# Optimization experiments

Hardware: AMD Instinct MI355X
Metric: run time of the kernel (lower is better)

The kernel has to match this reference:

```python
import jax, jax.numpy as jnp
import numpy as np

B, T, Dx, H, K = 32, 4096, 128, 128, 10


def setup_inputs() -> dict:
    key = jax.random.key(0)
    ks = jax.random.split(key, 11)
    s = 1.0 / np.sqrt(H)  # PyTorch GRU init range

    def p(k, shape):
        return jax.random.uniform(k, shape, jnp.float32, -s, s)

    return {
        "x": jax.random.normal(ks[0], (B, T, Dx), jnp.float32),
        # forward-direction GRU params (gate order: r, z, n as in PyTorch)
        "W_ih_f": p(ks[1], (3 * H, Dx)),
        "W_hh_f": p(ks[2], (3 * H, H)),
        "b_ih_f": p(ks[3], (3 * H,)),
        "b_hh_f": p(ks[4], (3 * H,)),
        # backward-direction GRU params
        "W_ih_b": p(ks[5], (3 * H, Dx)),
        "W_hh_b": p(ks[6], (3 * H, H)),
        "b_ih_b": p(ks[7], (3 * H,)),
        "b_hh_b": p(ks[8], (3 * H,)),
        # final linear classifier
        "W_fc": p(ks[9], (K, 2 * H)),
        "b_fc": p(ks[10], (K,)),
    }


def _gru_scan(x, Wih, Whh, bih, bhh, reverse):
    """Single-direction GRU over time. x: [B,T,Dx] -> [B,T,H]."""
    # Precompute all input projections at once: [T, B, 3H]
    xp = jnp.einsum('btd,gd->tbg', x, Wih) + bih
    Whh_T = Whh.T
    Hd = Whh.shape[1]

    def cell(h, xt):
        hp = h @ Whh_T + bhh            # [B, 3H]
        xr, xz, xn = jnp.split(xt, 3, axis=-1)
        hr, hz, hn = jnp.split(hp, 3, axis=-1)
        r = jax.nn.sigmoid(xr + hr)
        z = jax.nn.sigmoid(xz + hz)
        n = jnp.tanh(xn + r * hn)
        h_new = (1.0 - z) * n + z * h
        return h_new, h_new

    h0 = jnp.zeros((x.shape[0], Hd), x.dtype)
    _, hs = jax.lax.scan(cell, h0, xp, reverse=reverse)  # [T, B, H]
    return jnp.transpose(hs, (1, 0, 2))


def reference(x, W_ih_f, W_hh_f, b_ih_f, b_hh_f,
              W_ih_b, W_hh_b, b_ih_b, b_hh_b, W_fc, b_fc):
    hf = _gru_scan(x, W_ih_f, W_hh_f, b_ih_f, b_hh_f, reverse=False)
    hb = _gru_scan(x, W_ih_b, W_hh_b, b_ih_b, b_hh_b, reverse=True)
    h = jnp.concatenate([hf, hb], axis=-1)  # [B, T, 2H]
    return h @ W_fc.T + b_fc                # [B, T, K]
```

## Files before the change

kernel.cpp:

```cpp
#include <hip/hip_runtime.h>
#include <cstdint>
#include <cstddef>

#define T_LEN   4096
#define B_SZ    32
#define H_DIM   128
#define DX      128
#define K_CLS   10
#define CHUNK   32
#define NCHUNKS (T_LEN / CHUNK)
#define XA_LD   136
#define HIST_LD 136

typedef _Float16 half2v  __attribute__((ext_vector_type(2)));
typedef _Float16 half8   __attribute__((ext_vector_type(8)));
typedef float    floatx4 __attribute__((ext_vector_type(4)));

__device__ __forceinline__ float dot2f(unsigned int w, unsigned int h, float acc) {
  return __builtin_amdgcn_fdot2(__builtin_bit_cast(half2v, w),
                                __builtin_bit_cast(half2v, h), acc, false);
}

__device__ __forceinline__ unsigned int packh2(float a, float b) {
  half2v h;
  h.x = (_Float16)a;
  h.y = (_Float16)b;
  return __builtin_bit_cast(unsigned int, h);
}

__device__ __forceinline__ float dpp_xor1_add(float x) {
  int xi = __builtin_bit_cast(int, x);
  int yi = __builtin_amdgcn_update_dpp(xi, xi, 0xB1, 0xF, 0xF, false);
  return x + __builtin_bit_cast(float, yi);
}

__device__ __forceinline__ float sigm(float x) {
  x = fminf(fmaxf(x, -30.f), 30.f);
  return __builtin_amdgcn_rcpf(1.f + __expf(-x));
}

__device__ __forceinline__ float tanhfast(float x) {
  x = fminf(fmaxf(x, -15.f), 15.f);
  float t = __expf(-2.f * x);
  return (1.f - t) * __builtin_amdgcn_rcpf(1.f + t);
}

__global__ void __launch_bounds__(256) init_out_kernel(float* __restrict__ out,
                                                       const float* __restrict__ bfc) {
  int i = blockIdx.x * 256 + threadIdx.x;
  if (i < B_SZ * T_LEN * K_CLS) out[i] = bfc[i % K_CLS];
}

__global__ void __launch_bounds__(256, 1)
gru_bidir_kernel(const float* __restrict__ x,
                 const float* __restrict__ Wih_f, const float* __restrict__ Whh_f,
                 const float* __restrict__ bih_f, const float* __restrict__ bhh_f,
                 const float* __restrict__ Wih_b, const float* __restrict__ Whh_b,
                 const float* __restrict__ bih_b, const float* __restrict__ bhh_b,
                 const float* __restrict__ Wfc, float* __restrict__ out) {
  const int tid = threadIdx.x;
  const int bid = blockIdx.x;
  const int b   = bid & (B_SZ - 1);
  const int dir = bid >> 5;

  const float* Wih = dir ? Wih_b : Wih_f;
  const float* Whh = dir ? Whh_b : Whh_f;
  const float* bih = dir ? bih_b : bih_f;
  const float* bhh = dir ? bhh_b : bhh_f;

  const int lane = tid & 63;
  const int wv   = tid >> 6;
  const int col  = lane & 15;
  const int quad = lane >> 4;
  const int j    = tid >> 1;
  const int q    = tid & 1;

  __shared__ __align__(16) _Float16 xA[CHUNK][XA_LD];
  __shared__ __align__(16) _Float16 xh2[CHUNK][4 * H_DIM];
  __shared__ __align__(16) _Float16 hist[CHUNK][HIST_LD];
  __shared__ __align__(16) _Float16 hbuf[2][H_DIM];

  unsigned int whr[32], whz[32], whn[32];
  {
    const float* Wr = Whh + (size_t)j * H_DIM + q * 64;
    const float* Wz = Whh + (size_t)(H_DIM + j) * H_DIM + q * 64;
    const float* Wn = Whh + (size_t)(2 * H_DIM + j) * H_DIM + q * 64;
#pragma unroll
    for (int i = 0; i < 32; ++i) {
      whr[i] = packh2(Wr[2 * i], Wr[2 * i + 1]);
      whz[i] = packh2(Wz[2 * i], Wz[2 * i + 1]);
      whn[i] = packh2(Wn[2 * i], Wn[2 * i + 1]);
    }
  }
  const float cbr  = bih[j] + bhh[j];
  const float cbz  = bih[H_DIM + j] + bhh[H_DIM + j];
  const float bin_ = bih[2 * H_DIM + j];
  const float bhn  = bhh[2 * H_DIM + j];

  half8 fcfrag[4];
#pragma unroll
  for (int ks = 0; ks < 4; ++ks) {
    half8 v;
#pragma unroll
    for (int e = 0; e < 8; ++e) {
      int cc = ks * 32 + quad * 8 + e;
      v[e] = (col < K_CLS) ? (_Float16)Wfc[(size_t)col * (2 * H_DIM) + dir * H_DIM + cc]
                           : (_Float16)0.f;
    }
    fcfrag[ks] = v;
  }

  if (tid < 128) hbuf[0][tid] = (_Float16)0.f;

  const int s_row = tid >> 3;
  const int cbase = (tid & 7) * 16;
  float4 px0, px1, px2, px3;
  {
    int t0 = dir ? (T_LEN - 1 - s_row) : s_row;
    const float* xp = x + ((size_t)b * T_LEN + t0) * DX + cbase;
    px0 = *(const float4*)xp;       px1 = *(const float4*)(xp + 4);
    px2 = *(const float4*)(xp + 8); px3 = *(const float4*)(xp + 12);
  }

  float hold = 0.f;
  __syncthreads();

  for (int c = 0; c < NCHUNKS; ++c) {
    {
      half8 lo, hi;
      lo[0] = (_Float16)px0.x; lo[1] = (_Float16)px0.y; lo[2] = (_Float16)px0.z; lo[3] = (_Float16)px0.w;
      lo[4] = (_Float16)px1.x; lo[5] = (_Float16)px1.y; lo[6] = (_Float16)px1.z; lo[7] = (_Float16)px1.w;
      hi[0] = (_Float16)px2.x; hi[1] = (_Float16)px2.y; hi[2] = (_Float16)px2.z; hi[3] = (_Float16)px2.w;
      hi[4] = (_Float16)px3.x; hi[5] = (_Float16)px3.y; hi[6] = (_Float16)px3.z; hi[7] = (_Float16)px3.w;
      *(half8*)&xA[s_row][cbase] = lo;
      *(half8*)&xA[s_row][cbase + 8] = hi;
    }
    __syncthreads();

#pragma unroll
    for (int nt = 0; nt < 6; ++nt) {
      const int g = (wv * 6 + nt) * 16 + col;
      const float* wsrc = Wih + (size_t)g * DX + quad * 8;
      half8 bf[4];
#pragma unroll
      for (int ks = 0; ks < 4; ++ks) {
        const float* s8 = wsrc + ks * 32;
        half8 v;
#pragma unroll
        for (int e = 0; e < 8; ++e) v[e] = (_Float16)s8[e];
        bf[ks] = v;
      }
      floatx4 a0 = (floatx4){0.f, 0.f, 0.f, 0.f};
      floatx4 a1 = (floatx4){0.f, 0.f, 0.f, 0.f};
#pragma unroll
      for (int ks = 0; ks < 4; ++ks) {
        half8 af0 = *(const half8*)&xA[col][ks * 32 + quad * 8];
        half8 af1 = *(const half8*)&xA[16 + col][ks * 32 + quad * 8];
        a0 = __builtin_amdgcn_mfma_f32_16x16x32_f16(af0, bf[ks], a0, 0, 0, 0);
        a1 = __builtin_amdgcn_mfma_f32_16x16x32_f16(af1, bf[ks], a1, 0, 0, 0);
      }
      const int jj = (g & 127) * 4 + (g >> 7);
#pragma unroll
      for (int i = 0; i < 4; ++i) {
        xh2[quad * 4 + i][jj]      = (_Float16)a0[i];
        xh2[16 + quad * 4 + i][jj] = (_Float16)a1[i];
      }
    }

    if (c + 1 < NCHUNKS) {
      int s = (c + 1) * CHUNK + s_row;
      int t0 = dir ? (T_LEN - 1 - s) : s;
      const float* xp = x + ((size_t)b * T_LEN + t0) * DX + cbase;
      px0 = *(const float4*)xp;       px1 = *(const float4*)(xp + 4);
      px2 = *(const float4*)(xp + 8); px3 = *(const float4*)(xp + 12);
    }
    __syncthreads();

    int p = 0;
#pragma unroll 2
    for (int s = 0; s < CHUNK; ++s) {
      const uint2 xv = *(const uint2*)&xh2[s][j * 4];
      const uint4* hb = (const uint4*)&hbuf[p][q * 64];
      uint4 h0 = hb[0], h1 = hb[1], h2 = hb[2], h3 = hb[3];
      uint4 h4 = hb[4], h5 = hb[5], h6 = hb[6], h7 = hb[7];
      unsigned int hh[32];
      hh[0]=h0.x;  hh[1]=h0.y;  hh[2]=h0.z;  hh[3]=h0.w;
      hh[4]=h1.x;  hh[5]=h1.y;  hh[6]=h1.z;  hh[7]=h1.w;
      hh[8]=h2.x;  hh[9]=h2.y;  hh[10]=h2.z; hh[11]=h2.w;
      hh[12]=h3.x; hh[13]=h3.y; hh[14]=h3.z; hh[15]=h3.w;
      hh[16]=h4.x; hh[17]=h4.y; hh[18]=h4.z; hh[19]=h4.w;
      hh[20]=h5.x; hh[21]=h5.y; hh[22]=h5.z; hh[23]=h5.w;
      hh[24]=h6.x; hh[25]=h6.y; hh[26]=h6.z; hh[27]=h6.w;
      hh[28]=h7.x; hh[29]=h7.y; hh[30]=h7.z; hh[31]=h7.w;

      float ar0 = 0.f, ar1 = 0.f, az0 = 0.f, az1 = 0.f, an0 = 0.f, an1 = 0.f;
#pragma unroll
      for (int i = 0; i < 16; ++i) {
        ar0 = dot2f(whr[2 * i],     hh[2 * i],     ar0);
        ar1 = dot2f(whr[2 * i + 1], hh[2 * i + 1], ar1);
        az0 = dot2f(whz[2 * i],     hh[2 * i],     az0);
        az1 = dot2f(whz[2 * i + 1], hh[2 * i + 1], az1);
        an0 = dot2f(whn[2 * i],     hh[2 * i],     an0);
        an1 = dot2f(whn[2 * i + 1], hh[2 * i + 1], an1);
      }
      float ar = dpp_xor1_add(ar0 + ar1);
      float az = dpp_xor1_add(az0 + az1);
      float an = dpp_xor1_add(an0 + an1);

      half2v x01 = __builtin_bit_cast(half2v, xv.x);
      half2v x23 = __builtin_bit_cast(half2v, xv.y);
      float rr = sigm((float)x01.x + cbr + ar);
      float zz = sigm((float)x01.y + cbz + az);
      float nn = tanhfast((float)x23.x + bin_ + rr * (an + bhn));
      hold = nn + zz * (hold - nn);

      if (q == 0) {
        _Float16 hf = (_Float16)hold;
        hbuf[p ^ 1][j] = hf;
        hist[s][j] = hf;
      }
      p ^= 1;
      __syncthreads();
    }

    if (wv < 2) {
      const int mt = wv;
      floatx4 facc = (floatx4){0.f, 0.f, 0.f, 0.f};
#pragma unroll
      for (int ks = 0; ks < 4; ++ks) {
        half8 af = *(const half8*)&hist[mt * 16 + col][ks * 32 + quad * 8];
        facc = __builtin_amdgcn_mfma_f32_16x16x32_f16(af, fcfrag[ks], facc, 0, 0, 0);
      }
      if (col < K_CLS) {
#pragma unroll
        for (int i = 0; i < 4; ++i) {
          int s = mt * 16 + quad * 4 + i;
          int t = c * CHUNK + s;
          int tt = dir ? (T_LEN - 1 - t) : t;
          atomicAdd(out + ((size_t)b * T_LEN + tt) * K_CLS + col, facc[i]);
        }
      }
    }
  }
}

extern "C" void kernel_launch(void* const* d_in, const int* in_sizes, int n_in,
                              void* d_out, int out_size, void* d_ws, size_t ws_size,
                              hipStream_t stream) {
  (void)in_sizes; (void)n_in; (void)d_ws; (void)ws_size; (void)out_size;
  const float* x     = (const float*)d_in[0];
  const float* Wih_f = (const float*)d_in[1];
  const float* Whh_f = (const float*)d_in[2];
  const float* bih_f = (const float*)d_in[3];
  const float* bhh_f = (const float*)d_in[4];
  const float* Wih_b = (const float*)d_in[5];
  const float* Whh_b = (const float*)d_in[6];
  const float* bih_b = (const float*)d_in[7];
  const float* bhh_b = (const float*)d_in[8];
  const float* Wfc   = (const float*)d_in[9];
  const float* bfc   = (const float*)d_in[10];
  float* out = (float*)d_out;

  const int n_out = B_SZ * T_LEN * K_CLS;
  init_out_kernel<<<(n_out + 255) / 256, 256, 0, stream>>>(out, bfc);
  gru_bidir_kernel<<<B_SZ * 2, 256, 0, stream>>>(x, Wih_f, Whh_f, bih_f, bhh_f,
                                                 Wih_b, Whh_b, bih_b, bhh_b, Wfc, out);
}
```

Baseline: 2.008 ms.

## Process four batch rows per block with interleaved recurrence steps

Each workgroup now carries four batch sequences of one direction (16 blocks instead of 64), with the time chunk cut from 32 to 8. Within each time step the four independent GRU updates are interleaved, so their dot products and LDS loads can hide each other's latency, and one barrier per step is shared by four sequences. A separate pre-kernel converts W_ih to fp16 once in the workspace so the chunk projection loads half-precision weights directly. Barriers are replaced by an explicit lgkmcnt wait plus s_barrier. The trade-off is four times the serial work per step on far fewer compute units.

```diff
diff --git a/kernel.cpp b/kernel.cpp
--- a/kernel.cpp
+++ b/kernel.cpp
@@ -7,10 +7,13 @@
 #define H_DIM   128
 #define DX      128
 #define K_CLS   10
-#define CHUNK   32
+#define G       4
+#define CHUNK   8
+#define NROW    (G * CHUNK)
 #define NCHUNKS (T_LEN / CHUNK)
 #define XA_LD   136
-#define HIST_LD 136
+#define HI_LD   136
+#define XH_W    520
 
 typedef _Float16 half2v  __attribute__((ext_vector_type(2)));
 typedef _Float16 half8   __attribute__((ext_vector_type(8)));
@@ -45,40 +48,56 @@
   return (1.f - t) * __builtin_amdgcn_rcpf(1.f + t);
 }
 
+__device__ __forceinline__ void bar_lgkm() {
+  asm volatile("s_waitcnt lgkmcnt(0)\n\ts_barrier" ::: "memory");
+}
+
 __global__ void __launch_bounds__(256) init_out_kernel(float* __restrict__ out,
                                                        const float* __restrict__ bfc) {
   int i = blockIdx.x * 256 + threadIdx.x;
   if (i < B_SZ * T_LEN * K_CLS) out[i] = bfc[i % K_CLS];
 }
 
+__global__ void __launch_bounds__(256) cvt_wih_kernel(const float* __restrict__ a,
+                                                      const float* __restrict__ b,
+                                                      _Float16* __restrict__ oa,
+                                                      _Float16* __restrict__ ob) {
+  int i = blockIdx.x * 256 + threadIdx.x;
+  if (i < 3 * H_DIM * DX) {
+    oa[i] = (_Float16)a[i];
+    ob[i] = (_Float16)b[i];
+  }
+}
+
 __global__ void __launch_bounds__(256, 1)
 gru_bidir_kernel(const float* __restrict__ x,
-                 const float* __restrict__ Wih_f, const float* __restrict__ Whh_f,
-                 const float* __restrict__ bih_f, const float* __restrict__ bhh_f,
-                 const float* __restrict__ Wih_b, const float* __restrict__ Whh_b,
-                 const float* __restrict__ bih_b, const float* __restrict__ bhh_b,
+                 const float* __restrict__ Whh_f, const float* __restrict__ bih_f,
+                 const float* __restrict__ bhh_f,
+                 const float* __restrict__ Whh_b, const float* __restrict__ bih_b,
+                 const float* __restrict__ bhh_b,
+                 const _Float16* __restrict__ wih16_f, const _Float16* __restrict__ wih16_b,
                  const float* __restrict__ Wfc, float* __restrict__ out) {
   const int tid = threadIdx.x;
   const int bid = blockIdx.x;
-  const int b   = bid & (B_SZ - 1);
-  const int dir = bid >> 5;
-
-  const float* Wih = dir ? Wih_b : Wih_f;
+  const int dir = bid >> 3;
+  const int b0  = (bid & 7) * G;
+
   const float* Whh = dir ? Whh_b : Whh_f;
   const float* bih = dir ? bih_b : bih_f;
   const float* bhh = dir ? bhh_b : bhh_f;
-
-  const int lane = tid & 63;
-  const int wv   = tid >> 6;
-  const int col  = lane & 15;
-  const int quad = lane >> 4;
-  const int j    = tid >> 1;
-  const int q    = tid & 1;
-
-  __shared__ __align__(16) _Float16 xA[CHUNK][XA_LD];
-  __shared__ __align__(16) _Float16 xh2[CHUNK][4 * H_DIM];
-  __shared__ __align__(16) _Float16 hist[CHUNK][HIST_LD];
-  __shared__ __align__(16) _Float16 hbuf[2][H_DIM];
+  const _Float16* Wih16 = dir ? wih16_b : wih16_f;
+
+  const int lane  = tid & 63;
+  const int wv    = tid >> 6;
+  const int mcol  = lane & 15;
+  const int mquad = lane >> 4;
+  const int j     = tid >> 1;
+  const int q     = tid & 1;
+
+  __shared__ __align__(16) _Float16 xAf[NROW * XA_LD];
+  __shared__ __align__(16) _Float16 xh2f[NROW * XH_W];
+  __shared__ __align__(16) _Float16 histf[NROW * HI_LD];
+  __shared__ __align__(16) _Float16 hbuf[2][G][H_DIM];
 
   unsigned int whr[32], whz[32], whn[32];
   {
@@ -103,124 +122,148 @@
     half8 v;
 #pragma unroll
     for (int e = 0; e < 8; ++e) {
-      int cc = ks * 32 + quad * 8 + e;
-      v[e] = (col < K_CLS) ? (_Float16)Wfc[(size_t)col * (2 * H_DIM) + dir * H_DIM + cc]
-                           : (_Float16)0.f;
+      int cc = ks * 32 + mquad * 8 + e;
+      v[e] = (mcol < K_CLS) ? (_Float16)Wfc[(size_t)mcol * (2 * H_DIM) + dir * H_DIM + cc]
+                            : (_Float16)0.f;
     }
     fcfrag[ks] = v;
   }
 
-  if (tid < 128) hbuf[0][tid] = (_Float16)0.f;
-
-  const int s_row = tid >> 3;
+  if (tid < 128) {
+#pragma unroll
+    for (int c = 0; c < G; ++c) hbuf[0][c][tid] = (_Float16)0.f;
+  }
+
+  const int prow  = tid >> 3;
+  const int pc    = prow >> 3;
+  const int ps    = prow & 7;
   const int cbase = (tid & 7) * 16;
   float4 px0, px1, px2, px3;
   {
-    int t0 = dir ? (T_LEN - 1 - s_row) : s_row;
-    const float* xp = x + ((size_t)b * T_LEN + t0) * DX + cbase;
+    int t0 = dir ? (T_LEN - 1 - ps) : ps;
+    const float* xp = x + ((size_t)(b0 + pc) * T_LEN + t0) * DX + cbase;
     px0 = *(const float4*)xp;       px1 = *(const float4*)(xp + 4);
     px2 = *(const float4*)(xp + 8); px3 = *(const float4*)(xp + 12);
   }
 
-  float hold = 0.f;
+  float hold0 = 0.f, hold1 = 0.f, hold2 = 0.f, hold3 = 0.f;
+  int p = 0;
   __syncthreads();
 
-  for (int c = 0; c < NCHUNKS; ++c) {
+  auto ldhh = [&](int c, uint4* h) {
+    const uint4* hb = (const uint4*)&hbuf[p][c][q * 64];
+#pragma unroll
+    for (int i = 0; i < 8; ++i) h[i] = hb[i];
+  };
+  auto ldxv = [&](int c, int s) -> uint2 {
+    return *(const uint2*)&xh2f[(size_t)(c * CHUNK + s) * XH_W + j * 4];
+  };
+  auto stepc = [&](int c, int s, const uint4* hv, uint2 xv, float hold) -> float {
+    unsigned int hh[32];
+#pragma unroll
+    for (int i = 0; i < 8; ++i) {
+      hh[4 * i]     = hv[i].x;
+      hh[4 * i + 1] = hv[i].y;
+      hh[4 * i + 2] = hv[i].z;
+      hh[4 * i + 3] = hv[i].w;
+    }
+    float ar0 = 0.f, ar1 = 0.f, az0 = 0.f, az1 = 0.f, an0 = 0.f, an1 = 0.f;
+#pragma unroll
+    for (int i = 0; i < 16; ++i) {
+      ar0 = dot2f(whr[2 * i],     hh[2 * i],     ar0);
+      ar1 = dot2f(whr[2 * i + 1], hh[2 * i + 1], ar1);
+      az0 = dot2f(whz[2 * i],     hh[2 * i],     az0);
+      az1 = dot2f(whz[2 * i + 1], hh[2 * i + 1], az1);
+      an0 = dot2f(whn[2 * i],     hh[2 * i],     an0);
+      an1 = dot2f(whn[2 * i + 1], hh[2 * i + 1], an1);
+    }
+    float ar = dpp_xor1_add(ar0 + ar1);
+    float az = dpp_xor1_add(az0 + az1);
+    float an = dpp_xor1_add(an0 + an1);
+
+    half2v x01 = __builtin_bit_cast(half2v, xv.x);
+    half2v x23 = __builtin_bit_cast(half2v, xv.y);
+    float rr = sigm((float)x01.x + cbr + ar);
+    float zz = sigm((float)x01.y + cbz + az);
+    float nn = tanhfast((float)x23.x + bin_ + rr * (an + bhn));
+    float hnew = nn + zz * (hold - nn);
+    if (q == 0) {
+      _Float16 hf = (_Float16)hnew;
+      hbuf[p ^ 1][c][j] = hf;
+      histf[(size_t)(c * CHUNK + s) * HI_LD + j] = hf;
+    }
+    return hnew;
+  };
+
+  for (int ck = 0; ck < NCHUNKS; ++ck) {
     {
       half8 lo, hi;
       lo[0] = (_Float16)px0.x; lo[1] = (_Float16)px0.y; lo[2] = (_Float16)px0.z; lo[3] = (_Float16)px0.w;
       lo[4] = (_Float16)px1.x; lo[5] = (_Float16)px1.y; lo[6] = (_Float16)px1.z; lo[7] = (_Float16)px1.w;
       hi[0] = (_Float16)px2.x; hi[1] = (_Float16)px2.y; hi[2] = (_Float16)px2.z; hi[3] = (_Float16)px2.w;
       hi[4] = (_Float16)px3.x; hi[5] = (_Float16)px3.y; hi[6] = (_Float16)px3.z; hi[7] = (_Float16)px3.w;
-      *(half8*)&xA[s_row][cbase] = lo;
-      *(half8*)&xA[s_row][cbase + 8] = hi;
-    }
-    __syncthreads();
-
-#pragma unroll
-    for (int nt = 0; nt < 6; ++nt) {
-      const int g = (wv * 6 + nt) * 16 + col;
-      const float* wsrc = Wih + (size_t)g * DX + quad * 8;
-      half8 bf[4];
-#pragma unroll
-      for (int ks = 0; ks < 4; ++ks) {
-        const float* s8 = wsrc + ks * 32;
-        half8 v;
-#pragma unroll
-        for (int e = 0; e < 8; ++e) v[e] = (_Float16)s8[e];
-        bf[ks] = v;
-      }
-      floatx4 a0 = (floatx4){0.f, 0.f, 0.f, 0.f};
-      floatx4 a1 = (floatx4){0.f, 0.f, 0.f, 0.f};
-#pragma unroll
-      for (int ks = 0; ks < 4; ++ks) {
-        half8 af0 = *(const half8*)&xA[col][ks * 32 + quad * 8];
-        half8 af1 = *(const half8*)&xA[16 + col][ks * 32 + quad * 8];
-        a0 = __builtin_amdgcn_mfma_f32_16x16x32_f16(af0, bf[ks], a0, 0, 0, 0);
-        a1 = __builtin_amdgcn_mfma_f32_16x16x32_f16(af1, bf[ks], a1, 0, 0, 0);
-      }
-      const int jj = (g & 127) * 4 + (g >> 7);
-#pragma unroll
-      for (int i = 0; i < 4; ++i) {
-        xh2[quad * 4 + i][jj]      = (_Float16)a0[i];
-        xh2[16 + quad * 4 + i][jj] = (_Float16)a1[i];
-      }
-    }
-
-    if (c + 1 < NCHUNKS) {
-      int s = (c + 1) * CHUNK + s_row;
-      int t0 = dir ? (T_LEN - 1 - s) : s;
-      const float* xp = x + ((size_t)b * T_LEN + t0) * DX + cbase;
-      px0 = *(const float4*)xp;       px1 = *(const float4*)(xp + 4);
-      px2 = *(const float4*)(xp + 8); px3 = *(const float4*)(xp + 12);
-    }
-    __syncthreads();
-
-    int p = 0;
-#pragma unroll 2
+      *(half8*)&xAf[prow * XA_LD + cbase] = lo;
+      *(half8*)&xAf[prow * XA_LD + cbase + 8] = hi;
+    }
+    bar_lgkm();
+
+    {
+      floatx4 acc[6][2];
+#pragma unroll
+      for (int nt = 0; nt < 6; ++nt) {
+        acc[nt][0] = (floatx4){0.f, 0.f, 0.f, 0.f};
+        acc[nt][1] = (floatx4){0.f, 0.f, 0.f, 0.f};
+      }
+#pragma unroll
+      for (int nt = 0; nt < 6; ++nt) {
+        const int g = (wv * 6 + nt) * 16 + mcol;
+        const _Float16* wsrc = Wih16 + (size_t)g * DX + mquad * 8;
+        half8 bf0 = *(const half8*)(wsrc);
+        half8 bf1 = *(const half8*)(wsrc + 32);
+        half8 bf2 = *(const half8*)(wsrc + 64);
+        half8 bf3 = *(const half8*)(wsrc + 96);
+#pragma unroll
+        for (int mt = 0; mt < 2; ++mt) {
+          const _Float16* ab = &xAf[(mt * 16 + mcol) * XA_LD + mquad * 8];
+          acc[nt][mt] = __builtin_amdgcn_mfma_f32_16x16x32_f16(*(const half8*)(ab),      bf0, acc[nt][mt], 0, 0, 0);
+          acc[nt][mt] = __builtin_amdgcn_mfma_f32_16x16x32_f16(*(const half8*)(ab + 32), bf1, acc[nt][mt], 0, 0, 0);
+          acc[nt][mt] = __builtin_amdgcn_mfma_f32_16x16x32_f16(*(const half8*)(ab + 64), bf2, acc[nt][mt], 0, 0, 0);
+          acc[nt][mt] = __builtin_amdgcn_mfma_f32_16x16x32_f16(*(const half8*)(ab + 96), bf3, acc[nt][mt], 0, 0, 0);
+        }
+      }
+
+      if (ck + 1 < NCHUNKS) {
+        int t = (ck + 1) * CHUNK + ps;
+        int t0 = dir ? (T_LEN - 1 - t) : t;
+        const float* xp = x + ((size_t)(b0 + pc) * T_LEN + t0) * DX + cbase;
+        px0 = *(const float4*)xp;       px1 = *(const float4*)(xp + 4);
+        px2 = *(const float4*)(xp + 8); px3 = *(const float4*)(xp + 12);
+      }
+
+#pragma unroll
+      for (int nt = 0; nt < 6; ++nt) {
+        const int g  = (wv * 6 + nt) * 16 + mcol;
+        const int jj = (g & 127) * 4 + (g >> 7);
+#pragma unroll
+        for (int mt = 0; mt < 2; ++mt)
+#pragma unroll
+          for (int i = 0; i < 4; ++i)
+            xh2f[(size_t)(mt * 16 + mquad * 4 + i) * XH_W + jj] = (_Float16)acc[nt][mt][i];
+      }
+    }
+    bar_lgkm();
+
+#pragma unroll 1
     for (int s = 0; s < CHUNK; ++s) {
-      const uint2 xv = *(const uint2*)&xh2[s][j * 4];
-      const uint4* hb = (const uint4*)&hbuf[p][q * 64];
-      uint4 h0 = hb[0], h1 = hb[1], h2 = hb[2], h3 = hb[3];
-      uint4 h4 = hb[4], h5 = hb[5], h6 = hb[6], h7 = hb[7];
-      unsigned int hh[32];
-      hh[0]=h0.x;  hh[1]=h0.y;  hh[2]=h0.z;  hh[3]=h0.w;
-      hh[4]=h1.x;  hh[5]=h1.y;  hh[6]=h1.z;  hh[7]=h1.w;
-      hh[8]=h2.x;  hh[9]=h2.y;  hh[10]=h2.z; hh[11]=h2.w;
-      hh[12]=h3.x; hh[13]=h3.y; hh[14]=h3.z; hh[15]=h3.w;
-      hh[16]=h4.x; hh[17]=h4.y; hh[18]=h4.z; hh[19]=h4.w;
-      hh[20]=h5.x; hh[21]=h5.y; hh[22]=h5.z; hh[23]=h5.w;
-      hh[24]=h6.x; hh[25]=h6.y; hh[26]=h6.z; hh[27]=h6.w;
-      hh[28]=h7.x; hh[29]=h7.y; hh[30]=h7.z; hh[31]=h7.w;
-
-      float ar0 = 0.f, ar1 = 0.f, az0 = 0.f, az1 = 0.f, an0 = 0.f, an1 = 0.f;
-#pragma unroll
-      for (int i = 0; i < 16; ++i) {
-        ar0 = dot2f(whr[2 * i],     hh[2 * i],     ar0);
-        ar1 = dot2f(whr[2 * i + 1], hh[2 * i + 1], ar1);
-        az0 = dot2f(whz[2 * i],     hh[2 * i],     az0);
-        az1 = dot2f(whz[2 * i + 1], hh[2 * i + 1], az1);
-        an0 = dot2f(whn[2 * i],     hh[2 * i],     an0);
-        an1 = dot2f(whn[2 * i + 1], hh[2 * i + 1], an1);
-      }
-      float ar = dpp_xor1_add(ar0 + ar1);
-      float az = dpp_xor1_add(az0 + az1);
-      float an = dpp_xor1_add(an0 + an1);
-
-      half2v x01 = __builtin_bit_cast(half2v, xv.x);
-      half2v x23 = __builtin_bit_cast(half2v, xv.y);
-      float rr = sigm((float)x01.x + cbr + ar);
-      float zz = sigm((float)x01.y + cbz + az);
-      float nn = tanhfast((float)x23.x + bin_ + rr * (an + bhn));
-      hold = nn + zz * (hold - nn);
-
-      if (q == 0) {
-        _Float16 hf = (_Float16)hold;
-        hbuf[p ^ 1][j] = hf;
-        hist[s][j] = hf;
-      }
+      uint4 hA[8], hB[8];
+      ldhh(0, hA); uint2 xv0 = ldxv(0, s);
+      ldhh(1, hB); uint2 xv1 = ldxv(1, s);
+      hold0 = stepc(0, s, hA, xv0, hold0); ldhh(2, hA); uint2 xv2 = ldxv(2, s);
+      hold1 = stepc(1, s, hB, xv1, hold1); ldhh(3, hB); uint2 xv3 = ldxv(3, s);
+      hold2 = stepc(2, s, hA, xv2, hold2);
+      hold3 = stepc(3, s, hB, xv3, hold3);
       p ^= 1;
-      __syncthreads();
+      bar_lgkm();
     }
 
     if (wv < 2) {
@@ -228,16 +271,17 @@
       floatx4 facc = (floatx4){0.f, 0.f, 0.f, 0.f};
 #pragma unroll
       for (int ks = 0; ks < 4; ++ks) {
-        half8 af = *(const half8*)&hist[mt * 16 + col][ks * 32 + quad * 8];
+        half8 af = *(const half8*)&histf[(size_t)(mt * 16 + mcol) * HI_LD + ks * 32 + mquad * 8];
         facc = __builtin_amdgcn_mfma_f32_16x16x32_f16(af, fcfrag[ks], facc, 0, 0, 0);
       }
-      if (col < K_CLS) {
+      if (mcol < K_CLS) {
 #pragma unroll
         for (int i = 0; i < 4; ++i) {
-          int s = mt * 16 + quad * 4 + i;
-          int t = c * CHUNK + s;
+          int r  = mt * 16 + mquad * 4 + i;
+          int cc = r >> 3, ss = r & 7;
+          int t  = ck * CHUNK + ss;
           int tt = dir ? (T_LEN - 1 - t) : t;
-          atomicAdd(out + ((size_t)b * T_LEN + tt) * K_CLS + col, facc[i]);
+          atomicAdd(out + ((size_t)(b0 + cc) * T_LEN + tt) * K_CLS + mcol, facc[i]);
         }
       }
     }
@@ -247,7 +291,7 @@
 extern "C" void kernel_launch(void* const* d_in, const int* in_sizes, int n_in,
                               void* d_out, int out_size, void* d_ws, size_t ws_size,
                               hipStream_t stream) {
-  (void)in_sizes; (void)n_in; (void)d_ws; (void)ws_size; (void)out_size;
+  (void)in_sizes; (void)n_in; (void)ws_size; (void)out_size;
   const float* x     = (const float*)d_in[0];
   const float* Wih_f = (const float*)d_in[1];
   const float* Whh_f = (const float*)d_in[2];
@@ -261,8 +305,14 @@
   const float* bfc   = (const float*)d_in[10];
   float* out = (float*)d_out;
 
+  _Float16* wih16_f = (_Float16*)d_ws;
+  _Float16* wih16_b = wih16_f + 3 * H_DIM * DX;
+
   const int n_out = B_SZ * T_LEN * K_CLS;
+  const int n_w   = 3 * H_DIM * DX;
   init_out_kernel<<<(n_out + 255) / 256, 256, 0, stream>>>(out, bfc);
-  gru_bidir_kernel<<<B_SZ * 2, 256, 0, stream>>>(x, Wih_f, Whh_f, bih_f, bhh_f,
-                                                 Wih_b, Whh_b, bih_b, bhh_b, Wfc, out);
-}
+  cvt_wih_kernel<<<(n_w + 255) / 256, 256, 0, stream>>>(Wih_f, Wih_b, wih16_f, wih16_b);
+  gru_bidir_kernel<<<(B_SZ * 2) / G, 256, 0, stream>>>(x, Whh_f, bih_f, bhh_f,
+                                                       Whh_b, bih_b, bhh_b,
+                                                       wih16_f, wih16_b, Wfc, out);
+}
```

Result: slower. 7.984 ms (+297.6%).

## Move GRU recurrent matvec to MFMA and pre-convert weights to fp16

Applied to the files above, without the earlier changes.

The per-step hidden-state projection switches from per-thread fdot2 accumulation over register-held weights to MFMA 16x16x32 instructions. The hidden vector sits in row 0 of a zero-padded 16-row LDS tile, and each wave holds Whh B-fragments in registers for two 16-column slices of each gate. A small pre-kernel converts all input and recurrent weights to fp16 in workspace, which removes the per-chunk fp32-to-fp16 conversion of Wih. Barriers become a raw lgkmcnt wait plus s_barrier. The padded MFMA does 16x redundant work and leaves a serial dependent MFMA chain on the critical path of every step, so per-step latency may rise.

```diff
diff --git a/kernel.cpp b/kernel.cpp
--- a/kernel.cpp
+++ b/kernel.cpp
@@ -9,30 +9,15 @@
 #define K_CLS   10
 #define CHUNK   32
 #define NCHUNKS (T_LEN / CHUNK)
+#define WMAT    (3 * H_DIM * DX)
 #define XA_LD   136
-#define HIST_LD 136
+#define XP_LD   520
+#define HI_LD   136
+#define HA_LD   136
 
 typedef _Float16 half2v  __attribute__((ext_vector_type(2)));
 typedef _Float16 half8   __attribute__((ext_vector_type(8)));
 typedef float    floatx4 __attribute__((ext_vector_type(4)));
-
-__device__ __forceinline__ float dot2f(unsigned int w, unsigned int h, float acc) {
-  return __builtin_amdgcn_fdot2(__builtin_bit_cast(half2v, w),
-                                __builtin_bit_cast(half2v, h), acc, false);
-}
-
-__device__ __forceinline__ unsigned int packh2(float a, float b) {
-  half2v h;
-  h.x = (_Float16)a;
-  h.y = (_Float16)b;
-  return __builtin_bit_cast(unsigned int, h);
-}
-
-__device__ __forceinline__ float dpp_xor1_add(float x) {
-  int xi = __builtin_bit_cast(int, x);
-  int yi = __builtin_amdgcn_update_dpp(xi, xi, 0xB1, 0xF, 0xF, false);
-  return x + __builtin_bit_cast(float, yi);
-}
 
 __device__ __forceinline__ float sigm(float x) {
   x = fminf(fmaxf(x, -30.f), 30.f);
@@ -45,57 +30,77 @@
   return (1.f - t) * __builtin_amdgcn_rcpf(1.f + t);
 }
 
+__device__ __forceinline__ void bar_lgkm() {
+  asm volatile("s_waitcnt lgkmcnt(0)\n\ts_barrier" ::: "memory");
+}
+
 __global__ void __launch_bounds__(256) init_out_kernel(float* __restrict__ out,
                                                        const float* __restrict__ bfc) {
   int i = blockIdx.x * 256 + threadIdx.x;
   if (i < B_SZ * T_LEN * K_CLS) out[i] = bfc[i % K_CLS];
 }
 
+__global__ void __launch_bounds__(256) cvt_w_kernel(const float* __restrict__ a,
+                                                    const float* __restrict__ b,
+                                                    const float* __restrict__ c,
+                                                    const float* __restrict__ d,
+                                                    _Float16* __restrict__ o) {
+  int i = blockIdx.x * 256 + threadIdx.x;
+  if (i < WMAT) {
+    o[i]            = (_Float16)a[i];
+    o[WMAT + i]     = (_Float16)b[i];
+    o[2 * WMAT + i] = (_Float16)c[i];
+    o[3 * WMAT + i] = (_Float16)d[i];
+  }
+}
+
 __global__ void __launch_bounds__(256, 1)
-gru_bidir_kernel(const float* __restrict__ x,
-                 const float* __restrict__ Wih_f, const float* __restrict__ Whh_f,
-                 const float* __restrict__ bih_f, const float* __restrict__ bhh_f,
-                 const float* __restrict__ Wih_b, const float* __restrict__ Whh_b,
-                 const float* __restrict__ bih_b, const float* __restrict__ bhh_b,
-                 const float* __restrict__ Wfc, float* __restrict__ out) {
+gru_scan_kernel(const float* __restrict__ x,
+                const float* __restrict__ bih_f, const float* __restrict__ bhh_f,
+                const float* __restrict__ bih_b, const float* __restrict__ bhh_b,
+                const _Float16* __restrict__ w16,
+                const float* __restrict__ Wfc, float* __restrict__ out) {
   const int tid = threadIdx.x;
   const int bid = blockIdx.x;
+  const int dir = bid >> 5;
   const int b   = bid & (B_SZ - 1);
-  const int dir = bid >> 5;
-
-  const float* Wih = dir ? Wih_b : Wih_f;
-  const float* Whh = dir ? Whh_b : Whh_f;
+
   const float* bih = dir ? bih_b : bih_f;
   const float* bhh = dir ? bhh_b : bhh_f;
+  const _Float16* Wih16 = w16 + (size_t)dir * WMAT;
+  const _Float16* Whh16 = w16 + (size_t)(2 + dir) * WMAT;
 
   const int lane = tid & 63;
   const int wv   = tid >> 6;
   const int col  = lane & 15;
   const int quad = lane >> 4;
-  const int j    = tid >> 1;
-  const int q    = tid & 1;
-
-  __shared__ __align__(16) _Float16 xA[CHUNK][XA_LD];
-  __shared__ __align__(16) _Float16 xh2[CHUNK][4 * H_DIM];
-  __shared__ __align__(16) _Float16 hist[CHUNK][HIST_LD];
-  __shared__ __align__(16) _Float16 hbuf[2][H_DIM];
-
-  unsigned int whr[32], whz[32], whn[32];
-  {
-    const float* Wr = Whh + (size_t)j * H_DIM + q * 64;
-    const float* Wz = Whh + (size_t)(H_DIM + j) * H_DIM + q * 64;
-    const float* Wn = Whh + (size_t)(2 * H_DIM + j) * H_DIM + q * 64;
-#pragma unroll
-    for (int i = 0; i < 32; ++i) {
-      whr[i] = packh2(Wr[2 * i], Wr[2 * i + 1]);
-      whz[i] = packh2(Wz[2 * i], Wz[2 * i + 1]);
-      whn[i] = packh2(Wn[2 * i], Wn[2 * i + 1]);
-    }
-  }
-  const float cbr  = bih[j] + bhh[j];
-  const float cbz  = bih[H_DIM + j] + bhh[H_DIM + j];
-  const float bin_ = bih[2 * H_DIM + j];
-  const float bhn  = bhh[2 * H_DIM + j];
+
+  __shared__ __align__(16) _Float16 xAf[CHUNK * XA_LD];
+  __shared__ __align__(16) _Float16 xpL[CHUNK * XP_LD];
+  __shared__ __align__(16) _Float16 histf[CHUNK * HI_LD];
+  __shared__ __align__(16) _Float16 hA[2 * 16 * HA_LD];
+
+  half8 wb[6][4];
+#pragma unroll
+  for (int l = 0; l < 6; ++l) {
+    const int g  = l % 3;
+    const int jt = wv + 4 * (l / 3);
+    const int n  = g * 128 + jt * 16 + col;
+    const _Float16* src = Whh16 + (size_t)n * H_DIM + quad * 8;
+#pragma unroll
+    for (int ks = 0; ks < 4; ++ks) wb[l][ks] = *(const half8*)(src + ks * 32);
+  }
+
+  const int j1 = wv * 16 + col;
+  const int j2 = j1 + 64;
+  const float cbr1 = bih[j1] + bhh[j1];
+  const float cbz1 = bih[H_DIM + j1] + bhh[H_DIM + j1];
+  const float bin1 = bih[2 * H_DIM + j1];
+  const float bhn1 = bhh[2 * H_DIM + j1];
+  const float cbr2 = bih[j2] + bhh[j2];
+  const float cbz2 = bih[H_DIM + j2] + bhh[H_DIM + j2];
+  const float bin2 = bih[2 * H_DIM + j2];
+  const float bhn2 = bhh[2 * H_DIM + j2];
 
   half8 fcfrag[4];
 #pragma unroll
@@ -110,132 +115,132 @@
     fcfrag[ks] = v;
   }
 
-  if (tid < 128) hbuf[0][tid] = (_Float16)0.f;
-
-  const int s_row = tid >> 3;
+  {
+    unsigned int* hz = (unsigned int*)hA;
+    for (int i = tid; i < (2 * 16 * HA_LD) / 2; i += 256) hz[i] = 0u;
+  }
+
+  const int prow  = tid >> 3;
   const int cbase = (tid & 7) * 16;
   float4 px0, px1, px2, px3;
   {
-    int t0 = dir ? (T_LEN - 1 - s_row) : s_row;
+    int t0 = dir ? (T_LEN - 1 - prow) : prow;
     const float* xp = x + ((size_t)b * T_LEN + t0) * DX + cbase;
     px0 = *(const float4*)xp;       px1 = *(const float4*)(xp + 4);
     px2 = *(const float4*)(xp + 8); px3 = *(const float4*)(xp + 12);
   }
 
-  float hold = 0.f;
+  float hold1 = 0.f, hold2 = 0.f;
   __syncthreads();
 
-  for (int c = 0; c < NCHUNKS; ++c) {
+  for (int ck = 0; ck < NCHUNKS; ++ck) {
     {
       half8 lo, hi;
       lo[0] = (_Float16)px0.x; lo[1] = (_Float16)px0.y; lo[2] = (_Float16)px0.z; lo[3] = (_Float16)px0.w;
       lo[4] = (_Float16)px1.x; lo[5] = (_Float16)px1.y; lo[6] = (_Float16)px1.z; lo[7] = (_Float16)px1.w;
       hi[0] = (_Float16)px2.x; hi[1] = (_Float16)px2.y; hi[2] = (_Float16)px2.z; hi[3] = (_Float16)px2.w;
       hi[4] = (_Float16)px3.x; hi[5] = (_Float16)px3.y; hi[6] = (_Float16)px3.z; hi[7] = (_Float16)px3.w;
-      *(half8*)&xA[s_row][cbase] = lo;
-      *(half8*)&xA[s_row][cbase + 8] = hi;
-    }
-    __syncthreads();
-
-#pragma unroll
-    for (int nt = 0; nt < 6; ++nt) {
-      const int g = (wv * 6 + nt) * 16 + col;
-      const float* wsrc = Wih + (size_t)g * DX + quad * 8;
-      half8 bf[4];
+      *(half8*)&xAf[prow * XA_LD + cbase] = lo;
+      *(half8*)&xAf[prow * XA_LD + cbase + 8] = hi;
+    }
+    bar_lgkm();
+
+    {
+#pragma unroll
+      for (int nt = 0; nt < 6; ++nt) {
+        const int gg = (wv * 6 + nt) * 16 + col;
+        const _Float16* wsrc = Wih16 + (size_t)gg * DX + quad * 8;
+        half8 bf0 = *(const half8*)(wsrc);
+        half8 bf1 = *(const half8*)(wsrc + 32);
+        half8 bf2 = *(const half8*)(wsrc + 64);
+        half8 bf3 = *(const half8*)(wsrc + 96);
+        floatx4 a0 = (floatx4){0.f, 0.f, 0.f, 0.f};
+        floatx4 a1 = (floatx4){0.f, 0.f, 0.f, 0.f};
+#pragma unroll
+        for (int mt = 0; mt < 2; ++mt) {
+          const _Float16* ab = &xAf[(mt * 16 + col) * XA_LD + quad * 8];
+          floatx4& ac = mt ? a1 : a0;
+          ac = __builtin_amdgcn_mfma_f32_16x16x32_f16(*(const half8*)(ab),      bf0, ac, 0, 0, 0);
+          ac = __builtin_amdgcn_mfma_f32_16x16x32_f16(*(const half8*)(ab + 32), bf1, ac, 0, 0, 0);
+          ac = __builtin_amdgcn_mfma_f32_16x16x32_f16(*(const half8*)(ab + 64), bf2, ac, 0, 0, 0);
+          ac = __builtin_amdgcn_mfma_f32_16x16x32_f16(*(const half8*)(ab + 96), bf3, ac, 0, 0, 0);
+        }
+        const int jj = (gg & 127) * 4 + (gg >> 7);
+#pragma unroll
+        for (int i = 0; i < 4; ++i) {
+          xpL[(quad * 4 + i) * XP_LD + jj]        = (_Float16)a0[i];
+          xpL[(16 + quad * 4 + i) * XP_LD + jj]   = (_Float16)a1[i];
+        }
+      }
+
+      if (ck + 1 < NCHUNKS) {
+        int t = (ck + 1) * CHUNK + prow;
+        int t0 = dir ? (T_LEN - 1 - t) : t;
+        const float* xp = x + ((size_t)b * T_LEN + t0) * DX + cbase;
+        px0 = *(const float4*)xp;       px1 = *(const float4*)(xp + 4);
+        px2 = *(const float4*)(xp + 8); px3 = *(const float4*)(xp + 12);
+      }
+    }
+    bar_lgkm();
+
+    int p = 0;
+#pragma unroll 1
+    for (int s = 0; s < CHUNK; ++s) {
+      const _Float16* hrow = &hA[p * 16 * HA_LD + col * HA_LD + quad * 8];
+      half8 a0 = *(const half8*)(hrow);
+      half8 a1 = *(const half8*)(hrow + 32);
+      half8 a2 = *(const half8*)(hrow + 64);
+      half8 a3 = *(const half8*)(hrow + 96);
+      uint2 xv1 = *(const uint2*)&xpL[s * XP_LD + j1 * 4];
+      uint2 xv2 = *(const uint2*)&xpL[s * XP_LD + j2 * 4];
+
+      floatx4 acc[6];
+#pragma unroll
+      for (int l = 0; l < 6; ++l) acc[l] = (floatx4){0.f, 0.f, 0.f, 0.f};
+#pragma unroll
+      for (int l = 0; l < 6; ++l) {
+        acc[l] = __builtin_amdgcn_mfma_f32_16x16x32_f16(a0, wb[l][0], acc[l], 0, 0, 0);
+        acc[l] = __builtin_amdgcn_mfma_f32_16x16x32_f16(a1, wb[l][1], acc[l], 0, 0, 0);
+        acc[l] = __builtin_amdgcn_mfma_f32_16x16x32_f16(a2, wb[l][2], acc[l], 0, 0, 0);
+        acc[l] = __builtin_amdgcn_mfma_f32_16x16x32_f16(a3, wb[l][3], acc[l], 0, 0, 0);
+      }
+
+      if (quad == 0) {
+        half2v xa1 = __builtin_bit_cast(half2v, xv1.x);
+        half2v xb1 = __builtin_bit_cast(half2v, xv1.y);
+        half2v xa2 = __builtin_bit_cast(half2v, xv2.x);
+        half2v xb2 = __builtin_bit_cast(half2v, xv2.y);
+        float rr1 = sigm((float)xa1.x + cbr1 + acc[0][0]);
+        float zz1 = sigm((float)xa1.y + cbz1 + acc[1][0]);
+        float rr2 = sigm((float)xa2.x + cbr2 + acc[3][0]);
+        float zz2 = sigm((float)xa2.y + cbz2 + acc[4][0]);
+        float nn1 = tanhfast((float)xb1.x + bin1 + rr1 * (acc[2][0] + bhn1));
+        float nn2 = tanhfast((float)xb2.x + bin2 + rr2 * (acc[5][0] + bhn2));
+        hold1 = nn1 + zz1 * (hold1 - nn1);
+        hold2 = nn2 + zz2 * (hold2 - nn2);
+        _Float16 h1 = (_Float16)hold1;
+        _Float16 h2 = (_Float16)hold2;
+        hA[(p ^ 1) * 16 * HA_LD + j1] = h1;
+        hA[(p ^ 1) * 16 * HA_LD + j2] = h2;
+        histf[s * HI_LD + j1] = h1;
+        histf[s * HI_LD + j2] = h2;
+      }
+      p ^= 1;
+      bar_lgkm();
+    }
+
+    if (wv < 2) {
+      floatx4 facc = (floatx4){0.f, 0.f, 0.f, 0.f};
 #pragma unroll
       for (int ks = 0; ks < 4; ++ks) {
-        const float* s8 = wsrc + ks * 32;
-        half8 v;
-#pragma unroll
-        for (int e = 0; e < 8; ++e) v[e] = (_Float16)s8[e];
-        bf[ks] = v;
-      }
-      floatx4 a0 = (floatx4){0.f, 0.f, 0.f, 0.f};
-      floatx4 a1 = (floatx4){0.f, 0.f, 0.f, 0.f};
-#pragma unroll
-      for (int ks = 0; ks < 4; ++ks) {
-        half8 af0 = *(const half8*)&xA[col][ks * 32 + quad * 8];
-        half8 af1 = *(const half8*)&xA[16 + col][ks * 32 + quad * 8];
-        a0 = __builtin_amdgcn_mfma_f32_16x16x32_f16(af0, bf[ks], a0, 0, 0, 0);
-        a1 = __builtin_amdgcn_mfma_f32_16x16x32_f16(af1, bf[ks], a1, 0, 0, 0);
-      }
-      const int jj = (g & 127) * 4 + (g >> 7);
-#pragma unroll
-      for (int i = 0; i < 4; ++i) {
-        xh2[quad * 4 + i][jj]      = (_Float16)a0[i];
-        xh2[16 + quad * 4 + i][jj] = (_Float16)a1[i];
-      }
-    }
-
-    if (c + 1 < NCHUNKS) {
-      int s = (c + 1) * CHUNK + s_row;
-      int t0 = dir ? (T_LEN - 1 - s) : s;
-      const float* xp = x + ((size_t)b * T_LEN + t0) * DX + cbase;
-      px0 = *(const float4*)xp;       px1 = *(const float4*)(xp + 4);
-      px2 = *(const float4*)(xp + 8); px3 = *(const float4*)(xp + 12);
-    }
-    __syncthreads();
-
-    int p = 0;
-#pragma unroll 2
-    for (int s = 0; s < CHUNK; ++s) {
-      const uint2 xv = *(const uint2*)&xh2[s][j * 4];
-      const uint4* hb = (const uint4*)&hbuf[p][q * 64];
-      uint4 h0 = hb[0], h1 = hb[1], h2 = hb[2], h3 = hb[3];
-      uint4 h4 = hb[4], h5 = hb[5], h6 = hb[6], h7 = hb[7];
-      unsigned int hh[32];
-      hh[0]=h0.x;  hh[1]=h0.y;  hh[2]=h0.z;  hh[3]=h0.w;
-      hh[4]=h1.x;  hh[5]=h1.y;  hh[6]=h1.z;  hh[7]=h1.w;
-      hh[8]=h2.x;  hh[9]=h2.y;  hh[10]=h2.z; hh[11]=h2.w;
-      hh[12]=h3.x; hh[13]=h3.y; hh[14]=h3.z; hh[15]=h3.w;
-      hh[16]=h4.x; hh[17]=h4.y; hh[18]=h4.z; hh[19]=h4.w;
-      hh[20]=h5.x; hh[21]=h5.y; hh[22]=h5.z; hh[23]=h5.w;
-      hh[24]=h6.x; hh[25]=h6.y; hh[26]=h6.z; hh[27]=h6.w;
-      hh[28]=h7.x; hh[29]=h7.y; hh[30]=h7.z; hh[31]=h7.w;
-
-      float ar0 = 0.f, ar1 = 0.f, az0 = 0.f, az1 = 0.f, an0 = 0.f, an1 = 0.f;
-#pragma unroll
-      for (int i = 0; i < 16; ++i) {
-        ar0 = dot2f(whr[2 * i],     hh[2 * i],     ar0);
-        ar1 = dot2f(whr[2 * i + 1], hh[2 * i + 1], ar1);
-        az0 = dot2f(whz[2 * i],     hh[2 * i],     az0);
-        az1 = dot2f(whz[2 * i + 1], hh[2 * i + 1], az1);
-        an0 = dot2f(whn[2 * i],     hh[2 * i],     an0);
-        an1 = dot2f(whn[2 * i + 1], hh[2 * i + 1], an1);
-      }
-      float ar = dpp_xor1_add(ar0 + ar1);
-      float az = dpp_xor1_add(az0 + az1);
-      float an = dpp_xor1_add(an0 + an1);
-
-      half2v x01 = __builtin_bit_cast(half2v, xv.x);
-      half2v x23 = __builtin_bit_cast(half2v, xv.y);
-      float rr = sigm((float)x01.x + cbr + ar);
-      float zz = sigm((float)x01.y + cbz + az);
-      float nn = tanhfast((float)x23.x + bin_ + rr * (an + bhn));
-      hold = nn + zz * (hold - nn);
-
-      if (q == 0) {
-        _Float16 hf = (_Float16)hold;
-        hbuf[p ^ 1][j] = hf;
-        hist[s][j] = hf;
-      }
-      p ^= 1;
-      __syncthreads();
-    }
-
-    if (wv < 2) {
-      const int mt = wv;
-      floatx4 facc = (floatx4){0.f, 0.f, 0.f, 0.f};
-#pragma unroll
-      for (int ks = 0; ks < 4; ++ks) {
-        half8 af = *(const half8*)&hist[mt * 16 + col][ks * 32 + quad * 8];
+        half8 af = *(const half8*)&histf[(wv * 16 + col) * HI_LD + ks * 32 + quad * 8];
         facc = __builtin_amdgcn_mfma_f32_16x16x32_f16(af, fcfrag[ks], facc, 0, 0, 0);
       }
       if (col < K_CLS) {
 #pragma unroll
         for (int i = 0; i < 4; ++i) {
-          int s = mt * 16 + quad * 4 + i;
-          int t = c * CHUNK + s;
+          int s  = wv * 16 + quad * 4 + i;
+          int t  = ck * CHUNK + s;
           int tt = dir ? (T_LEN - 1 - t) : t;
           atomicAdd(out + ((size_t)b * T_LEN + tt) * K_CLS + col, facc[i]);
         }
@@ -247,7 +252,7 @@
 extern "C" void kernel_launch(void* const* d_in, const int* in_sizes, int n_in,
                               void* d_out, int out_size, void* d_ws, size_t ws_size,
                               hipStream_t stream) {
-  (void)in_sizes; (void)n_in; (void)d_ws; (void)ws_size; (void)out_size;
+  (void)in_sizes; (void)n_in; (void)ws_size; (void)out_size;
   const float* x     = (const float*)d_in[0];
   const float* Wih_f = (const float*)d_in[1];
   const float* Whh_f = (const float*)d_in[2];
@@ -261,8 +266,11 @@
   const float* bfc   = (const float*)d_in[10];
   float* out = (float*)d_out;
 
+  _Float16* w16 = (_Float16*)d_ws;
+
   const int n_out = B_SZ * T_LEN * K_CLS;
   init_out_kernel<<<(n_out + 255) / 256, 256, 0, stream>>>(out, bfc);
-  gru_bidir_kernel<<<B_SZ * 2, 256, 0, stream>>>(x, Wih_f, Whh_f, bih_f, bhh_f,
-                                                 Wih_b, Whh_b, bih_b, bhh_b, Wfc, out);
-}
+  cvt_w_kernel<<<(WMAT + 255) / 256, 256, 0, stream>>>(Wih_f, Wih_b, Whh_f, Whh_b, w16);
+  gru_scan_kernel<<<B_SZ * 2, 256, 0, stream>>>(x, bih_f, bhh_f, bih_b, bhh_b,
+                                                w16, Wfc, out);
+}
```

Result: slower. 2.408 ms (+20.0%).
